# Optimization experiments

Hardware: AMD Instinct MI355X
Metric: run time of the kernel (lower is better)

Reference implementation:

```python
import jax, jax.numpy as jnp
import numpy as np

D, M, N = 1024, 16, 16384
H = D // M  # head dim = 64
C = 10.0    # tanh logit clipping


def setup_inputs() -> dict:
    key = jax.random.key(0)
    kb, kq, km, k1, k2, k3, k4 = jax.random.split(key, 7)
    def xavier(k, shape):
        # torch xavier_uniform: fan_in = prod(shape[1:]), fan_out = shape[0]*prod(shape[2:])
        fan_in = int(np.prod(shape[1:]))
        fan_out = shape[0] * int(np.prod(shape[2:]))
        bound = float(np.sqrt(6.0 / (fan_in + fan_out)))
        return jax.random.uniform(k, shape, jnp.float32, -bound, bound)
    return {
        "b": jax.random.normal(kb, (N, D), jnp.float32),
        "q_s_bar": jax.random.normal(kq, (D,), jnp.float32),
        "mask": jax.random.randint(km, (N,), 0, 2).astype(bool),
        "W_k_bar": xavier(k1, (M, H, D)),
        "W_v_bar": xavier(k2, (M, H, D)),
        "W_k": xavier(k3, (D, D)),
        "W_q": xavier(k4, (D, D)),
    }


def reference(b, q_s_bar, mask, W_k_bar, W_v_bar, W_k, W_q):
    # k_bar, v_bar: (N, M, H)  == matmul(W, b.t()).permute(2,0,1)
    k_bar = jnp.einsum('mhd,nd->nmh', W_k_bar, b)
    v_bar = jnp.einsum('mhd,nd->nmh', W_v_bar, b)
    k = b @ W_k.T                      # (N, D) == matmul(W_k, b.t()).t()
    q = q_s_bar.reshape(M, H)          # (M, H)
    # c_bar: (N, M, M) == matmul(k_bar, q.T) / sqrt(h)
    c_bar = jnp.einsum('nmh,gh->nmg', k_bar, q) / np.float32(np.sqrt(H))
    scores = jnp.where(mask[:, None, None], c_bar, -jnp.inf)
    attn = jax.nn.softmax(scores, axis=0)          # softmax over N
    # (N,M,M) @ (N,M,H) batched -> (N,M,H); view(N,-1).sum(0) -> (D,)
    q_s = jnp.einsum('nmg,ngh->nmh', attn, v_bar).reshape(N, D).sum(0)
    c = (k @ (W_q @ q_s)) / np.float32(np.sqrt(D))  # (N,)
    c = C * jnp.tanh(c)
    return jnp.where(mask, c, -jnp.inf)
```

## Files before the change

kernel.cpp:

```cpp
#include <hip/hip_runtime.h>
#include <math.h>
#include <float.h>

#define NN 16384
#define DD 1024
#define MM 16
#define HH 64
#define MG 256

typedef __attribute__((ext_vector_type(8))) short bh8;
typedef __attribute__((ext_vector_type(4))) float f32x4;

__device__ inline float bf2f(unsigned short u) {
    union { unsigned int i; float f; } v;
    v.i = ((unsigned int)u) << 16;
    return v.f;
}

__device__ inline unsigned short f2bf(float f) {
    union { float f; unsigned int i; } v;
    v.f = f;
    unsigned int r = v.i + 0x7FFFu + ((v.i >> 16) & 1u);
    return (unsigned short)(r >> 16);
}

__device__ inline float ld1(const void* p, long i, int isf) {
    return isf ? ((const float*)p)[i] : bf2f(((const unsigned short*)p)[i]);
}

__device__ inline float4 ld4(const void* p, long i, int isf) {
    if (isf) return *(const float4*)((const float*)p + i);
    ushort4 u = *(const ushort4*)((const unsigned short*)p + i);
    return make_float4(bf2f(u.x), bf2f(u.y), bf2f(u.z), bf2f(u.w));
}

__device__ inline bool get_mask(const unsigned char* mp, int n, int flag) {
    return flag ? (mp[n] != 0) : (mp[4 * n] != 0);
}

__device__ inline void gl_lds16(const void* g, void* l) {
    __builtin_amdgcn_global_load_lds(
        (const __attribute__((address_space(1))) unsigned int*)g,
        (__attribute__((address_space(3))) unsigned int*)l, 16, 0, 0);
}

__global__ void detect(const unsigned char* __restrict__ mp,
                       const unsigned char* __restrict__ bb, int* flags,
                       float* __restrict__ u, float* __restrict__ l) {
    int i = blockIdx.x * 256 + threadIdx.x;
    if (i < DD) u[i] = 0.f;
    if (i < MG) l[i] = 0.f;
    int v1 = ((i & 3) != 0 && mp[i] != 0) ? 1 : 0;
    unsigned char c = bb[4 * i + 1];
    bool expish = (c == 0x00) || (c == 0x80) || (c >= 0x30 && c <= 0x47) ||
                  (c >= 0xB0 && c <= 0xC7);
    int v2 = expish ? 0 : 1;
    unsigned long long b1 = __ballot(v1);
    unsigned long long b2 = __ballot(v2);
    if ((threadIdx.x & 63) == 0) {
        if (b1) atomicOr(&flags[0], 1);
        if (b2) atomicOr(&flags[1], 1);
    }
}

__global__ __launch_bounds__(256) void prep(const void* __restrict__ bB,
                                            unsigned short* __restrict__ bbf,
                                            unsigned short* __restrict__ bT,
                                            const void* __restrict__ Wkb,
                                            const void* __restrict__ qsb,
                                            unsigned short* __restrict__ Abf,
                                            const int* __restrict__ flags) {
    __shared__ __align__(16) unsigned short tl[128 * 64];
    const int isf = flags[1];
    const int bid = blockIdx.x;
    const int t = threadIdx.x;

    if (bid < 2048) {
        const int n0 = (bid >> 4) * 128, d0 = (bid & 15) * 64;
        const int nc = t & 15, dq = t >> 4;
        ushort4 v[8];
        if (!isf) {
            const unsigned short* bs = (const unsigned short*)bB;
            const int lane = t & 63, w = t >> 6;
            const int r8 = lane >> 3, c = lane & 7;
#pragma unroll
            for (int i2 = 0; i2 < 4; i2++) {
                int nrow = i2 * 32 + w * 8 + r8;
                int s = (i2 * 4 + w) & 7;
                gl_lds16(&bs[(long)(n0 + nrow) * DD + d0 + ((c ^ s) << 3)],
                         &tl[(i2 * 32 + w * 8) * 64]);
            }
            __syncthreads();
#pragma unroll
            for (int k = 0; k < 8; k++) {
                int n = nc * 8 + k;
                int byteoff = n * 128 + (((dq >> 1) ^ (nc & 7)) << 4) + (dq & 1) * 8;
                v[k] = *(const ushort4*)((const char*)tl + byteoff);
            }
        } else {
            const float* bf = (const float*)bB;
#pragma unroll
            for (int k = 0; k < 8; k++) {
                int n = nc * 8 + k;
                float4 f = *(const float4*)&bf[(long)(n0 + n) * DD + d0 + dq * 4];
                ushort4 o;
                o.x = f2bf(f.x); o.y = f2bf(f.y); o.z = f2bf(f.z); o.w = f2bf(f.w);
                v[k] = o;
                *(ushort4*)&bbf[(long)(n0 + n) * DD + d0 + dq * 4] = o;
            }
        }
#pragma unroll
        for (int j = 0; j < 4; j++) {
            bh8 o;
#pragma unroll
            for (int k = 0; k < 8; k++) o[k] = (short)(&v[k].x)[j];
            *(bh8*)&bT[(long)(d0 + dq * 4 + j) * NN + n0 + nc * 8] = o;
        }
    } else {
        float* q = (float*)tl;
        int b2 = bid - 2048;
        int m = b2 >> 2;
        int d = (b2 & 3) * 256 + t;
        for (int i = t; i < DD; i += 256) q[i] = ld1(qsb, i, isf);
        __syncthreads();
        float acc[MM];
#pragma unroll
        for (int g = 0; g < MM; g++) acc[g] = 0.f;
        for (int h = 0; h < HH; h++) {
            float wv = ld1(Wkb, (long)(m * HH + h) * DD + d, isf);
#pragma unroll
            for (int g = 0; g < MM; g++) acc[g] += wv * q[g * HH + h];
        }
#pragma unroll
        for (int g = 0; g < MM; g++)
            Abf[(long)(m * MM + g) * DD + d] = f2bf(acc[g] * 0.125f);
    }
}

__global__ __launch_bounds__(256) void gemm_b_mfma(
    const unsigned short* __restrict__ Abf, const void* __restrict__ bB,
    const unsigned short* __restrict__ bbf,
    const unsigned char* __restrict__ mp, const int* __restrict__ flags,
    unsigned short* __restrict__ Cb, float* __restrict__ l) {
    __shared__ __align__(16) unsigned short As[64 * 128];
    __shared__ __align__(16) unsigned short Bs[64 * 128];
    __shared__ float lsum[64];
    const unsigned short* Bsrc = flags[1] ? bbf : (const unsigned short*)bB;
    int i = blockIdx.x;
    int xcd = i & 7, j = i >> 3;
    int mb = j & 3;
    int nsl = xcd | ((j >> 2) << 3);
    int m0 = mb * 64, n0 = nsl * 64;
    int t = threadIdx.x;
    int lane = t & 63, w = t >> 6;
    int wm = w >> 1, wn = w & 1;
    int r = lane & 15, q = lane >> 4;
    f32x4 acc[2][2] = {};
    for (int k0 = 0; k0 < DD; k0 += 128) {
#pragma unroll
        for (int i2 = 0; i2 < 4; i2++) {
            int L = (i2 * 4 + w) * 64 + lane;
            int row = L >> 4, c = (L & 15) ^ (row & 7);
            gl_lds16(&Abf[(long)(m0 + row) * DD + k0 + c * 8], &As[(i2 * 4 + w) * 512]);
        }
#pragma unroll
        for (int i2 = 0; i2 < 4; i2++) {
            int L = (i2 * 4 + w) * 64 + lane;
            int row = L >> 4, c = (L & 15) ^ (row & 7);
            gl_lds16(&Bsrc[(long)(n0 + row) * DD + k0 + c * 8], &Bs[(i2 * 4 + w) * 512]);
        }
        __syncthreads();
#pragma unroll
        for (int h = 0; h < 4; h++) {
            bh8 af[2], bfr[2];
#pragma unroll
            for (int fi = 0; fi < 2; fi++) {
                int row = wm * 32 + fi * 16 + r;
                int ck = (h * 4 + q) ^ (row & 7);
                af[fi] = *(const bh8*)&As[row * 128 + ck * 8];
            }
#pragma unroll
            for (int fj = 0; fj < 2; fj++) {
                int row = wn * 32 + fj * 16 + r;
                int ck = (h * 4 + q) ^ (row & 7);
                bfr[fj] = *(const bh8*)&Bs[row * 128 + ck * 8];
            }
#pragma unroll
            for (int fi = 0; fi < 2; fi++)
#pragma unroll
                for (int fj = 0; fj < 2; fj++)
                    acc[fi][fj] = __builtin_amdgcn_mfma_f32_16x16x32_bf16(
                        af[fi], bfr[fj], acc[fi][fj], 0, 0, 0);
        }
        __syncthreads();
    }
    if (t < 64) lsum[t] = 0.f;
    __syncthreads();
    int mflag = flags[0];
    float pv[2][2][4];
#pragma unroll
    for (int fj = 0; fj < 2; fj++) {
        int gn = n0 + wn * 32 + fj * 16 + r;
        bool mk = get_mask(mp, gn, mflag);
#pragma unroll
        for (int fi = 0; fi < 2; fi++)
#pragma unroll
            for (int reg = 0; reg < 4; reg++) {
                float e = mk ? expf(acc[fi][fj][reg] - 8.0f) : 0.f;
                int gm = m0 + wm * 32 + fi * 16 + q * 4 + reg;
                Cb[(long)gm * NN + gn] = f2bf(e);
                pv[fi][fj][reg] = e;
            }
    }
#pragma unroll
    for (int fi = 0; fi < 2; fi++)
#pragma unroll
        for (int reg = 0; reg < 4; reg++)
            atomicAdd(&lsum[wm * 32 + fi * 16 + q * 4 + reg],
                      pv[fi][0][reg] + pv[fi][1][reg]);
    __syncthreads();
    if (t < 64) atomicAdd(&l[m0 + t], lsum[t]);
}

__global__ __launch_bounds__(256) void gemm_d_mfma(
    const unsigned short* __restrict__ Cb, const unsigned short* __restrict__ bT,
    unsigned short* __restrict__ Tpart) {
    __shared__ __align__(16) unsigned short As[64 * 128];
    __shared__ __align__(16) unsigned short Bs[64 * 128];
    int i = blockIdx.x;
    int xcd = i & 7, j = i >> 3;
    int z = xcd | ((j >> 6) << 3);
    int inner = j & 63;
    int mb = inner >> 4, db = inner & 15;
    int m0 = mb * 64, d0 = db * 64;
    long kbase = (long)z * 1024;
    unsigned short* Cg = Tpart + (long)z * (MG * DD);
    int t = threadIdx.x;
    int lane = t & 63, w = t >> 6;
    int wm = w >> 1, wn = w & 1;
    int r = lane & 15, q = lane >> 4;
    f32x4 acc[2][2] = {};
    for (int k0 = 0; k0 < 1024; k0 += 128) {
#pragma unroll
        for (int i2 = 0; i2 < 4; i2++) {
            int L = (i2 * 4 + w) * 64 + lane;
            int row = L >> 4, c = (L & 15) ^ (row & 7);
            gl_lds16(&Cb[(long)(m0 + row) * NN + kbase + k0 + c * 8], &As[(i2 * 4 + w) * 512]);
        }
#pragma unroll
        for (int i2 = 0; i2 < 4; i2++) {
            int L = (i2 * 4 + w) * 64 + lane;
            int row = L >> 4, c = (L & 15) ^ (row & 7);
            gl_lds16(&bT[(long)(d0 + row) * NN + kbase + k0 + c * 8], &Bs[(i2 * 4 + w) * 512]);
        }
        __syncthreads();
#pragma unroll
        for (int h = 0; h < 4; h++) {
            bh8 af[2], bfr[2];
#pragma unroll
            for (int fi = 0; fi < 2; fi++) {
                int row = wm * 32 + fi * 16 + r;
                int ck = (h * 4 + q) ^ (row & 7);
                af[fi] = *(const bh8*)&As[row * 128 + ck * 8];
            }
#pragma unroll
            for (int fj = 0; fj < 2; fj++) {
                int row = wn * 32 + fj * 16 + r;
                int ck = (h * 4 + q) ^ (row & 7);
                bfr[fj] = *(const bh8*)&Bs[row * 128 + ck * 8];
            }
#pragma unroll
            for (int fi = 0; fi < 2; fi++)
#pragma unroll
                for (int fj = 0; fj < 2; fj++)
                    acc[fi][fj] = __builtin_amdgcn_mfma_f32_16x16x32_bf16(
                        af[fi], bfr[fj], acc[fi][fj], 0, 0, 0);
        }
        __syncthreads();
    }
#pragma unroll
    for (int fi = 0; fi < 2; fi++)
#pragma unroll
        for (int fj = 0; fj < 2; fj++)
#pragma unroll
            for (int reg = 0; reg < 4; reg++) {
                int gm = m0 + wm * 32 + fi * 16 + q * 4 + reg;
                int gd = d0 + wn * 32 + fj * 16 + r;
                Cg[(long)gm * DD + gd] = f2bf(acc[fi][fj][reg]);
            }
}

__global__ void reduce_T(const unsigned short* __restrict__ Tpart,
                         const float* __restrict__ l, float* __restrict__ T) {
    long i = (long)(blockIdx.x * 256 + threadIdx.x) * 8;
    int row = (int)(i >> 10);
    float li = l[row];
    float inv = (li > 0.f) ? 1.0f / li : 0.f;
    float s[8] = {};
#pragma unroll
    for (int c = 0; c < 16; c++) {
        bh8 v = *(const bh8*)&Tpart[(long)c * (MG * DD) + i];
#pragma unroll
        for (int j = 0; j < 8; j++) s[j] += bf2f((unsigned short)v[j]);
    }
#pragma unroll
    for (int j = 0; j < 8; j++) s[j] *= inv;
    *(float4*)&T[i] = make_float4(s[0], s[1], s[2], s[3]);
    *(float4*)&T[i + 4] = make_float4(s[4], s[5], s[6], s[7]);
}

__global__ void fold_v(const void* __restrict__ Wvb, const float* __restrict__ T,
                       float* __restrict__ qs, const int* __restrict__ flags) {
    int isf = flags[1];
    int w = threadIdx.x >> 6, lane = threadIdx.x & 63;
    int o = blockIdx.x * 4 + w;
    int m = o >> 6, h = o & 63;
    float s = 0.f;
    for (int g = 0; g < MM; g++) {
        const float* Trow = T + (long)(m * MM + g) * DD;
        long wbase = (long)(g * HH + h) * DD;
#pragma unroll
        for (int k = 0; k < 4; k++) {
            int d = lane * 4 + k * 256;
            float4 tv = *(const float4*)&Trow[d];
            float4 wv = ld4(Wvb, wbase + d, isf);
            s += wv.x * tv.x + wv.y * tv.y + wv.z * tv.z + wv.w * tv.w;
        }
    }
    for (int off = 32; off; off >>= 1) s += __shfl_down(s, off, 64);
    if (lane == 0) qs[o] = s;
}

__global__ void matvec_rows(const void* __restrict__ W, const float* __restrict__ x,
                            float* __restrict__ y, const int* __restrict__ flags) {
    int isf = flags[1];
    int lane = threadIdx.x & 63;
    int r = blockIdx.x * 4 + (threadIdx.x >> 6);
    long base = (long)r * DD;
    float s = 0.f;
#pragma unroll
    for (int k = 0; k < 4; k++) {
        int j = lane * 4 + k * 256;
        float4 wv = ld4(W, base + j, isf);
        float4 xv = *(const float4*)&x[j];
        s += wv.x * xv.x + wv.y * xv.y + wv.z * xv.z + wv.w * xv.w;
    }
    for (int off = 32; off; off >>= 1) s += __shfl_down(s, off, 64);
    if (lane == 0) y[r] = s;
}

__global__ void matvec_col(const void* __restrict__ Wk, const float* __restrict__ w1,
                           float* __restrict__ u, const int* __restrict__ flags) {
    __shared__ float xs[16];
    int isf = flags[1];
    int d = blockIdx.x * 256 + threadIdx.x;
    int i0 = blockIdx.y * 16;
    if (threadIdx.x < 16) xs[threadIdx.x] = w1[i0 + threadIdx.x];
    __syncthreads();
    float s = 0.f;
#pragma unroll
    for (int ii = 0; ii < 16; ii++) s += ld1(Wk, (long)(i0 + ii) * DD + d, isf) * xs[ii];
    atomicAdd(&u[d], s);
}

__global__ void final_k(const void* __restrict__ bB,
                        const unsigned short* __restrict__ bbf,
                        const float* __restrict__ u,
                        const unsigned char* __restrict__ mp, const int* __restrict__ flags,
                        void* __restrict__ out) {
    int mflag = flags[0];
    int isf = flags[1];
    const unsigned short* bbase = isf ? bbf : (const unsigned short*)bB;
    int n = blockIdx.x * 4 + (threadIdx.x >> 6);
    int lane = threadIdx.x & 63;
    const unsigned short* row = bbase + (long)n * DD;
    float s = 0.f;
#pragma unroll
    for (int k = 0; k < 4; k++) {
        int j = lane * 4 + k * 256;
        ushort4 v = *(const ushort4*)&row[j];
        float4 uu = *(const float4*)&u[j];
        s += bf2f(v.x) * uu.x + bf2f(v.y) * uu.y + bf2f(v.z) * uu.z + bf2f(v.w) * uu.w;
    }
    for (int off = 32; off; off >>= 1) s += __shfl_down(s, off, 64);
    if (lane == 0) {
        float c = 10.f * tanhf(s * (1.0f / 32.0f));
        bool mk = get_mask(mp, n, mflag);
        if (isf) {
            union { unsigned int i; float f; } vv;
            vv.i = mk ? (((unsigned int)f2bf(c)) << 16) : 0xFF7F0000u;
            ((float*)out)[n] = vv.f;
        } else {
            ((unsigned short*)out)[n] = mk ? f2bf(c) : (unsigned short)0xFF7F;
        }
    }
}

extern "C" void kernel_launch(void* const* d_in, const int* in_sizes, int n_in,
                              void* d_out, int out_size, void* d_ws, size_t ws_size,
                              hipStream_t stream) {
    const void* b = d_in[0];
    const void* qsb = d_in[1];
    const unsigned char* mp = (const unsigned char*)d_in[2];
    const void* Wkb = d_in[3];
    const void* Wvb = d_in[4];
    const void* Wk = d_in[5];
    const void* Wq = d_in[6];

    char* ws = (char*)d_ws;
    unsigned short* bbf = (unsigned short*)(ws);
    unsigned short* bT = (unsigned short*)(ws + (32u << 20));
    unsigned short* Cb = (unsigned short*)(ws + (64u << 20));
    unsigned short* Tpart = (unsigned short*)(ws + (72u << 20));
    unsigned short* Abf = (unsigned short*)(ws + (88u << 20));
    float* T = (float*)(ws + (89u << 20));
    float* small = (float*)(ws + (90u << 20));
    float* qs = small;
    float* w1 = qs + 1024;
    float* u = w1 + 1024;
    float* l = u + 1024;
    int* flags = (int*)(l + 256);

    hipMemsetAsync(flags, 0, 2 * sizeof(int), stream);

    detect<<<64, 256, 0, stream>>>(mp, (const unsigned char*)b, flags, u, l);
    prep<<<2112, 256, 0, stream>>>(b, bbf, bT, Wkb, qsb, Abf, flags);
    gemm_b_mfma<<<1024, 256, 0, stream>>>(Abf, b, bbf, mp, flags, Cb, l);
    gemm_d_mfma<<<1024, 256, 0, stream>>>(Cb, bT, Tpart);
    reduce_T<<<128, 256, 0, stream>>>(Tpart, l, T);
    fold_v<<<256, 256, 0, stream>>>(Wvb, T, qs, flags);
    matvec_rows<<<256, 256, 0, stream>>>(Wq, qs, w1, flags);
    matvec_col<<<dim3(4, 64), 256, 0, stream>>>(Wk, w1, u, flags);
    final_k<<<4096, 256, 0, stream>>>(b, bbf, u, mp, flags, d_out);
}
```

Before: 228.0 us.

## Widen prep transpose tiles to 128x128 and stage fp32 path through LDS

The transpose part of the prep kernel now handles 128x128 tiles instead of 128x64, halving its block count. Both the bf16 and fp32 input paths load rows into a shared-memory tile with an XOR swizzle, then emit transposed 16-byte stores. This replaces the async global-to-LDS copy and the fp32 path's strided direct reads. Per-thread loads shrink to 4-byte accesses in a 32-iteration loop, which may lower memory-level parallelism compared with the previous 16-byte loads.

```diff
diff --git a/kernel.cpp b/kernel.cpp
--- a/kernel.cpp
+++ b/kernel.cpp
@@ -70,55 +70,52 @@
                                             const void* __restrict__ qsb,
                                             unsigned short* __restrict__ Abf,
                                             const int* __restrict__ flags) {
-    __shared__ __align__(16) unsigned short tl[128 * 64];
+    __shared__ __align__(16) unsigned short tl[128 * 128];
     const int isf = flags[1];
     const int bid = blockIdx.x;
     const int t = threadIdx.x;
 
-    if (bid < 2048) {
-        const int n0 = (bid >> 4) * 128, d0 = (bid & 15) * 64;
-        const int nc = t & 15, dq = t >> 4;
-        ushort4 v[8];
-        if (!isf) {
-            const unsigned short* bs = (const unsigned short*)bB;
-            const int lane = t & 63, w = t >> 6;
-            const int r8 = lane >> 3, c = lane & 7;
-#pragma unroll
-            for (int i2 = 0; i2 < 4; i2++) {
-                int nrow = i2 * 32 + w * 8 + r8;
-                int s = (i2 * 4 + w) & 7;
-                gl_lds16(&bs[(long)(n0 + nrow) * DD + d0 + ((c ^ s) << 3)],
-                         &tl[(i2 * 32 + w * 8) * 64]);
-            }
-            __syncthreads();
+    if (bid < 1024) {
+        const int n0 = (bid >> 3) * 128, d0 = (bid & 7) * 128;
+        const int lane = t & 63, w = t >> 6;
+        for (int it = 0; it < 32; it++) {
+            int n = it * 4 + w;
+            int s4 = ((n >> 3) & 15) << 2;
+            int dl = lane * 2;
+            unsigned int packed;
+            if (isf) {
+                float2 f = *(const float2*)((const float*)bB +
+                                            (long)(n0 + n) * DD + d0 + dl);
+                packed = (unsigned int)f2bf(f.x) | ((unsigned int)f2bf(f.y) << 16);
+                *(unsigned int*)&bbf[(long)(n0 + n) * DD + d0 + dl] = packed;
+            } else {
+                packed = *(const unsigned int*)((const unsigned short*)bB +
+                                                (long)(n0 + n) * DD + d0 + dl);
+            }
+            *(unsigned int*)&tl[n * 128 + (dl ^ s4)] = packed;
+        }
+        __syncthreads();
+        const int nc = t & 15, dr = t >> 4;
+#pragma unroll
+        for (int p = 0; p < 2; p++) {
+            int dl = dr * 4 + p * 64;
+            ushort4 v[8];
 #pragma unroll
             for (int k = 0; k < 8; k++) {
                 int n = nc * 8 + k;
-                int byteoff = n * 128 + (((dq >> 1) ^ (nc & 7)) << 4) + (dq & 1) * 8;
-                v[k] = *(const ushort4*)((const char*)tl + byteoff);
-            }
-        } else {
-            const float* bf = (const float*)bB;
-#pragma unroll
-            for (int k = 0; k < 8; k++) {
-                int n = nc * 8 + k;
-                float4 f = *(const float4*)&bf[(long)(n0 + n) * DD + d0 + dq * 4];
-                ushort4 o;
-                o.x = f2bf(f.x); o.y = f2bf(f.y); o.z = f2bf(f.z); o.w = f2bf(f.w);
-                v[k] = o;
-                *(ushort4*)&bbf[(long)(n0 + n) * DD + d0 + dq * 4] = o;
-            }
-        }
-#pragma unroll
-        for (int j = 0; j < 4; j++) {
-            bh8 o;
-#pragma unroll
-            for (int k = 0; k < 8; k++) o[k] = (short)(&v[k].x)[j];
-            *(bh8*)&bT[(long)(d0 + dq * 4 + j) * NN + n0 + nc * 8] = o;
+                v[k] = *(const ushort4*)&tl[n * 128 + (dl ^ (nc << 2))];
+            }
+#pragma unroll
+            for (int j = 0; j < 4; j++) {
+                bh8 o;
+#pragma unroll
+                for (int k = 0; k < 8; k++) o[k] = (short)(&v[k].x)[j];
+                *(bh8*)&bT[(long)(d0 + dl + j) * NN + n0 + nc * 8] = o;
+            }
         }
     } else {
         float* q = (float*)tl;
-        int b2 = bid - 2048;
+        int b2 = bid - 1024;
         int m = b2 >> 2;
         int d = (b2 & 3) * 256 + t;
         for (int i = t; i < DD; i += 256) q[i] = ld1(qsb, i, isf);
@@ -424,7 +421,7 @@
     hipMemsetAsync(flags, 0, 2 * sizeof(int), stream);
 
     detect<<<64, 256, 0, stream>>>(mp, (const unsigned char*)b, flags, u, l);
-    prep<<<2112, 256, 0, stream>>>(b, bbf, bT, Wkb, qsb, Abf, flags);
+    prep<<<1088, 256, 0, stream>>>(b, bbf, bT, Wkb, qsb, Abf, flags);
     gemm_b_mfma<<<1024, 256, 0, stream>>>(Abf, b, bbf, mp, flags, Cb, l);
     gemm_d_mfma<<<1024, 256, 0, stream>>>(Cb, bT, Tpart);
     reduce_T<<<128, 256, 0, stream>>>(Tpart, l, T);
```

New measurement: 245.9 us. 1.08x slower.
